# Optimization experiments

Hardware: AMD Instinct MI355X
Metric: run time of the kernel (lower is better)

## Reference

```python
import jax, jax.numpy as jnp
import numpy as np

MARGIN = 0.5
TAU = 0.25
RHO = 10.0
SEMIHARD_LOSS_THRESHOLD = 0.0
EPS = 1e-12


def _pairwise_cosine_distances(x):
    # L2-normalize rows, distances = 1 - cosine similarity  -> [N, N]
    xn = x / jnp.maximum(jnp.linalg.norm(x, axis=1, keepdims=True), EPS)
    sim = xn @ xn.T
    dist = 1.0 - sim
    return dist, sim, xn


def _source_similarities(src):
    # distances normalized by their batch mean ('relative' / avg distances)
    dist, sim, xn = _pairwise_cosine_distances(src)
    avg_dist = dist / jnp.maximum(jnp.mean(dist), EPS)
    return dist, avg_dist, sim, xn


def _weights_from_distances(avg_dist, tau):
    # soft relaxed label weights from teacher distances
    pair_weights = jnp.exp(-avg_dist / tau)                      # [N, N] pos-pair weight
    neg_pair_weights = 1.0 - pair_weights                        # [N, N]
    # triplet (i, j=pos, k=neg): weight = w_pos[i,j] * w_neg[i,k]  -> [N, N, N]
    triplet_weights = pair_weights[:, :, None] * neg_pair_weights[:, None, :]
    return pair_weights, neg_pair_weights, triplet_weights


def _safe_division(num, den):
    return jnp.where(den > 0.0, num / jnp.where(den > 0.0, den, 1.0), 0.0)


def setup_inputs() -> dict:
    key = jax.random.key(0)
    k1, k2 = jax.random.split(key)
    N, D = 384, 128
    source_embeddings = jax.random.normal(k1, (N, D), dtype=jnp.float32)
    embeddings = jax.random.normal(k2, (N, D), dtype=jnp.float32)
    return {"source_embeddings": source_embeddings, "embeddings": embeddings}


def reference(source_embeddings, embeddings):
    src = jax.lax.stop_gradient(source_embeddings)  # .detach()
    _, source_avg_distances, _, _ = _source_similarities(src)
    source_pair_weights, _, source_triplet_weights = _weights_from_distances(
        source_avg_distances, TAU)

    distances, _, _ = _pairwise_cosine_distances(embeddings)  # [N, N]
    # tdd[i, j, k] = d[i, k] - d[i, j]
    triplet_distance_differences = distances[:, None, :] - distances[:, :, None]
    triplet_losses = jax.nn.relu(MARGIN - triplet_distance_differences)  # [N, N, N]

    semihard = ((triplet_losses > 0.0) & (triplet_losses <= MARGIN)).astype(
        triplet_losses.dtype) * source_triplet_weights
    positive_pair_semihard_losses = jnp.max(triplet_losses * semihard, axis=2)  # [N, N]

    if SEMIHARD_LOSS_THRESHOLD > 0.0:
        hard = (triplet_losses > MARGIN).astype(triplet_losses.dtype) * source_triplet_weights
        normalized = jnp.min(triplet_losses - RHO * hard, axis=2)
        positive_pair_hard_losses = (normalized + RHO) * (normalized < 0.0).astype(
            normalized.dtype)
    else:
        positive_pair_hard_losses = 0.0

    gate = (positive_pair_semihard_losses <= SEMIHARD_LOSS_THRESHOLD).astype(
        positive_pair_semihard_losses.dtype)
    positive_pair_losses = positive_pair_semihard_losses + gate * positive_pair_hard_losses

    loss = _safe_division(jnp.sum(positive_pair_losses * source_pair_weights),
                          jnp.sum(source_pair_weights))
    return loss
```

## Files before the change

### kernel.cpp

```cpp
#include <hip/hip_runtime.h>
#include <hip/hip_bf16.h>

#define N 384
#define D 128
#define TAU 0.25f
#define MARGIN 0.5f

__global__ __launch_bounds__(256) void k_gram(const float* __restrict__ xsrc,
                                              const float* __restrict__ xemb,
                                              float* __restrict__ dsrc,
                                              float* __restrict__ demb,
                                              float* __restrict__ tsum,
                                              float* __restrict__ accum) {
    __shared__ float At[D][34];
    __shared__ float Bt[D][34];
    __shared__ float inv_s[64];
    __shared__ float ps[4];
    int bid = blockIdx.x;
    int lin = threadIdx.x;
    if (bid == 0 && lin == 0) {
        accum[0] = 0.f; accum[1] = 0.f;
        ((unsigned int*)accum)[2] = 0u;
    }
    int mat = (bid >= 144) ? 1 : 0;
    int t2  = mat ? bid - 144 : bid;
    int bi = t2 / 12, bj = t2 % 12;
    const float* xn = mat ? xemb : xsrc;
    float* out      = mat ? demb : dsrc;

    int wv = lin >> 6, lane = lin & 63;
    #pragma unroll
    for (int rr = 0; rr < 16; ++rr) {
        int vr = wv * 16 + rr;
        int r  = vr & 31;
        int grow = ((vr >> 5) ? bj : bi) * 32 + r;
        float2 v = ((const float2*)(xn + (size_t)grow * D))[lane];
        float ss = v.x * v.x + v.y * v.y;
        #pragma unroll
        for (int o = 32; o > 0; o >>= 1) ss += __shfl_xor(ss, o);
        if (lane == 0) inv_s[vr] = 1.0f / fmaxf(sqrtf(ss), 1e-12f);
    }
    __syncthreads();

    #pragma unroll
    for (int l = 0; l < 4; ++l) {
        int idx = lin + l * 256;
        int row = idx >> 5;
        int c4  = idx & 31;
        float ia = inv_s[row], ib = inv_s[32 + row];
        float4 va = ((const float4*)(xn + (size_t)(bi * 32 + row) * D))[c4];
        At[c4 * 4 + 0][row] = va.x * ia; At[c4 * 4 + 1][row] = va.y * ia;
        At[c4 * 4 + 2][row] = va.z * ia; At[c4 * 4 + 3][row] = va.w * ia;
        float4 vb = ((const float4*)(xn + (size_t)(bj * 32 + row) * D))[c4];
        Bt[c4 * 4 + 0][row] = vb.x * ib; Bt[c4 * 4 + 1][row] = vb.y * ib;
        Bt[c4 * 4 + 2][row] = vb.z * ib; Bt[c4 * 4 + 3][row] = vb.w * ib;
    }
    __syncthreads();

    int tx = lin & 15, ty = lin >> 4;
    float a00 = 0.f, a01 = 0.f, a10 = 0.f, a11 = 0.f;
    #pragma unroll 8
    for (int k = 0; k < D; k++) {
        float x0 = At[k][2 * ty], x1 = At[k][2 * ty + 1];
        float y0 = Bt[k][2 * tx], y1 = Bt[k][2 * tx + 1];
        a00 = fmaf(x0, y0, a00); a01 = fmaf(x0, y1, a01);
        a10 = fmaf(x1, y0, a10); a11 = fmaf(x1, y1, a11);
    }
    float d00 = 1.f - a00, d01 = 1.f - a01, d10 = 1.f - a10, d11 = 1.f - a11;
    int r0 = bi * 32 + 2 * ty, c0 = bj * 32 + 2 * tx;
    out[(size_t)r0 * N + c0]           = d00;
    out[(size_t)r0 * N + c0 + 1]       = d01;
    out[(size_t)(r0 + 1) * N + c0]     = d10;
    out[(size_t)(r0 + 1) * N + c0 + 1] = d11;

    if (!mat) {
        float s = d00 + d01 + d10 + d11;
        #pragma unroll
        for (int o = 32; o > 0; o >>= 1) s += __shfl_xor(s, o);
        if ((lin & 63) == 0) ps[lin >> 6] = s;
        __syncthreads();
        if (lin == 0) tsum[t2] = ps[0] + ps[1] + ps[2] + ps[3];
    }
}

__global__ __launch_bounds__(N) void k_main(const float* __restrict__ dsrc,
                                            const float* __restrict__ demb,
                                            const float* __restrict__ tsum,
                                            float* __restrict__ accum,
                                            float* __restrict__ out) {
    __shared__ float wn[N];
    __shared__ float pn[6], pd[6];
    int i = blockIdx.x;
    int t = threadIdx.x;
    float total = 0.f;
    #pragma unroll
    for (int j = 0; j < 144; ++j) total += tsum[j];
    float mean  = total * (1.0f / (float)(N * N));
    float scale = 1.0f / (fmaxf(mean, 1e-12f) * TAU);
    const float* dsr = dsrc + (size_t)i * N;
    const float* der = demb + (size_t)i * N;
    float w = expf(-dsr[t] * scale);
    wn[t] = 1.0f - w;
    float c = MARGIN + der[t];
    __syncthreads();
    float m0 = 0.f, m1 = 0.f, m2 = 0.f, m3 = 0.f;
    #pragma unroll 2
    for (int k = 0; k < N; k += 4) {
        float4 wvk = *(const float4*)&wn[k];
        float d0 = der[k], d1 = der[k + 1], d2 = der[k + 2], d3 = der[k + 3];
        float tl0 = c - d0; float v0 = tl0 * wvk.x;
        v0 = (tl0 <= MARGIN) ? v0 : 0.f; m0 = fmaxf(m0, v0);
        float tl1 = c - d1; float v1 = tl1 * wvk.y;
        v1 = (tl1 <= MARGIN) ? v1 : 0.f; m1 = fmaxf(m1, v1);
        float tl2 = c - d2; float v2 = tl2 * wvk.z;
        v2 = (tl2 <= MARGIN) ? v2 : 0.f; m2 = fmaxf(m2, v2);
        float tl3 = c - d3; float v3 = tl3 * wvk.w;
        v3 = (tl3 <= MARGIN) ? v3 : 0.f; m3 = fmaxf(m3, v3);
    }
    float m = fmaxf(fmaxf(m0, m1), fmaxf(m2, m3));
    float numc = w * w * m;
    float denc = w;
    #pragma unroll
    for (int o = 32; o > 0; o >>= 1) {
        numc += __shfl_xor(numc, o);
        denc += __shfl_xor(denc, o);
    }
    if ((t & 63) == 0) { pn[t >> 6] = numc; pd[t >> 6] = denc; }
    __syncthreads();
    if (t == 0) {
        float sn = 0.f, sd = 0.f;
        #pragma unroll
        for (int wv = 0; wv < 6; wv++) { sn += pn[wv]; sd += pd[wv]; }
        atomicAdd(&accum[0], sn);
        atomicAdd(&accum[1], sd);
        __threadfence();
        unsigned int tk = atomicAdd((unsigned int*)accum + 2, 1u);
        if (tk == (unsigned int)(N - 1)) {
            float num = atomicAdd(&accum[0], 0.f);
            float den = atomicAdd(&accum[1], 0.f);
            out[0] = (den > 0.f) ? num / den : 0.f;
        }
    }
}

extern "C" void kernel_launch(void* const* d_in, const int* in_sizes, int n_in,
                              void* d_out, int out_size, void* d_ws, size_t ws_size,
                              hipStream_t stream) {
    const float* src = (const float*)d_in[0];
    const float* emb = (const float*)d_in[1];
    float* out = (float*)d_out;

    float* ws = (float*)d_ws;
    float* dsrc  = ws;
    float* demb  = dsrc + N * N;
    float* tsum  = demb + N * N;
    float* accum = tsum + 144;

    k_gram<<<288, 256, 0, stream>>>(src, emb, dsrc, demb, tsum, accum);
    k_main<<<N, N, 0, stream>>>(dsrc, demb, tsum, accum, out);
}
```

Before: 94.42 us.

## Fuse gram and main kernels into one persistent kernel with grid barriers

Merges the two launches into a single 384-block kernel that uses software grid barriers between phases: row normalization written to workspace, tiled Gram/distance computation, a grid-wide pass writing exp weights, then the per-row semihard max reduction. This removes a kernel launch boundary and the redundant per-tile norm recomputation. In exchange it adds a hipMemsetAsync, three global spin barriers, and extra global round-trips for normalized rows and weights. The barrier relies on all 384 blocks being co-resident, which could deadlock if they are not.

```diff
diff --git a/kernel.cpp b/kernel.cpp
--- a/kernel.cpp
+++ b/kernel.cpp
@@ -5,140 +5,160 @@
 #define D 128
 #define TAU 0.25f
 #define MARGIN 0.5f
+#define NBLK 384
 
-__global__ __launch_bounds__(256) void k_gram(const float* __restrict__ xsrc,
-                                              const float* __restrict__ xemb,
-                                              float* __restrict__ dsrc,
-                                              float* __restrict__ demb,
-                                              float* __restrict__ tsum,
-                                              float* __restrict__ accum) {
-    __shared__ float At[D][34];
-    __shared__ float Bt[D][34];
-    __shared__ float inv_s[64];
-    __shared__ float ps[4];
-    int bid = blockIdx.x;
-    int lin = threadIdx.x;
-    if (bid == 0 && lin == 0) {
-        accum[0] = 0.f; accum[1] = 0.f;
-        ((unsigned int*)accum)[2] = 0u;
-    }
-    int mat = (bid >= 144) ? 1 : 0;
-    int t2  = mat ? bid - 144 : bid;
-    int bi = t2 / 12, bj = t2 % 12;
-    const float* xn = mat ? xemb : xsrc;
-    float* out      = mat ? demb : dsrc;
+struct GramSh { float At[D][34]; float Bt[D][34]; float ps[4]; };
+struct MainSh { float pn[6]; float pd[6]; };
+union ShU { GramSh g; MainSh m; };
 
-    int wv = lin >> 6, lane = lin & 63;
-    #pragma unroll
-    for (int rr = 0; rr < 16; ++rr) {
-        int vr = wv * 16 + rr;
-        int r  = vr & 31;
-        int grow = ((vr >> 5) ? bj : bi) * 32 + r;
-        float2 v = ((const float2*)(xn + (size_t)grow * D))[lane];
-        float ss = v.x * v.x + v.y * v.y;
-        #pragma unroll
-        for (int o = 32; o > 0; o >>= 1) ss += __shfl_xor(ss, o);
-        if (lane == 0) inv_s[vr] = 1.0f / fmaxf(sqrtf(ss), 1e-12f);
+__device__ __forceinline__ void grid_bar(unsigned* bar, unsigned target) {
+    __syncthreads();
+    if (threadIdx.x == 0) {
+        __threadfence();
+        atomicAdd(bar, 1u);
+        while (__hip_atomic_load(bar, __ATOMIC_RELAXED,
+                                 __HIP_MEMORY_SCOPE_AGENT) < target) {
+            __builtin_amdgcn_s_sleep(2);
+        }
+        __threadfence();
     }
     __syncthreads();
-
-    #pragma unroll
-    for (int l = 0; l < 4; ++l) {
-        int idx = lin + l * 256;
-        int row = idx >> 5;
-        int c4  = idx & 31;
-        float ia = inv_s[row], ib = inv_s[32 + row];
-        float4 va = ((const float4*)(xn + (size_t)(bi * 32 + row) * D))[c4];
-        At[c4 * 4 + 0][row] = va.x * ia; At[c4 * 4 + 1][row] = va.y * ia;
-        At[c4 * 4 + 2][row] = va.z * ia; At[c4 * 4 + 3][row] = va.w * ia;
-        float4 vb = ((const float4*)(xn + (size_t)(bj * 32 + row) * D))[c4];
-        Bt[c4 * 4 + 0][row] = vb.x * ib; Bt[c4 * 4 + 1][row] = vb.y * ib;
-        Bt[c4 * 4 + 2][row] = vb.z * ib; Bt[c4 * 4 + 3][row] = vb.w * ib;
-    }
-    __syncthreads();
-
-    int tx = lin & 15, ty = lin >> 4;
-    float a00 = 0.f, a01 = 0.f, a10 = 0.f, a11 = 0.f;
-    #pragma unroll 8
-    for (int k = 0; k < D; k++) {
-        float x0 = At[k][2 * ty], x1 = At[k][2 * ty + 1];
-        float y0 = Bt[k][2 * tx], y1 = Bt[k][2 * tx + 1];
-        a00 = fmaf(x0, y0, a00); a01 = fmaf(x0, y1, a01);
-        a10 = fmaf(x1, y0, a10); a11 = fmaf(x1, y1, a11);
-    }
-    float d00 = 1.f - a00, d01 = 1.f - a01, d10 = 1.f - a10, d11 = 1.f - a11;
-    int r0 = bi * 32 + 2 * ty, c0 = bj * 32 + 2 * tx;
-    out[(size_t)r0 * N + c0]           = d00;
-    out[(size_t)r0 * N + c0 + 1]       = d01;
-    out[(size_t)(r0 + 1) * N + c0]     = d10;
-    out[(size_t)(r0 + 1) * N + c0 + 1] = d11;
-
-    if (!mat) {
-        float s = d00 + d01 + d10 + d11;
-        #pragma unroll
-        for (int o = 32; o > 0; o >>= 1) s += __shfl_xor(s, o);
-        if ((lin & 63) == 0) ps[lin >> 6] = s;
-        __syncthreads();
-        if (lin == 0) tsum[t2] = ps[0] + ps[1] + ps[2] + ps[3];
-    }
 }
 
-__global__ __launch_bounds__(N) void k_main(const float* __restrict__ dsrc,
-                                            const float* __restrict__ demb,
-                                            const float* __restrict__ tsum,
-                                            float* __restrict__ accum,
-                                            float* __restrict__ out) {
-    __shared__ float wn[N];
-    __shared__ float pn[6], pd[6];
-    int i = blockIdx.x;
+__global__ __launch_bounds__(NBLK) void k_fused(const float* __restrict__ xsrc,
+                                                const float* __restrict__ xemb,
+                                                float* __restrict__ xn_src,
+                                                float* __restrict__ xn_emb,
+                                                float* __restrict__ dsrc,
+                                                float* __restrict__ demb,
+                                                float* __restrict__ wsrc,
+                                                float* __restrict__ tsum,
+                                                float* __restrict__ accum,
+                                                float* __restrict__ out) {
+    __shared__ ShU sh;
+    int bid = blockIdx.x;
     int t = threadIdx.x;
-    float total = 0.f;
-    #pragma unroll
-    for (int j = 0; j < 144; ++j) total += tsum[j];
-    float mean  = total * (1.0f / (float)(N * N));
-    float scale = 1.0f / (fmaxf(mean, 1e-12f) * TAU);
-    const float* dsr = dsrc + (size_t)i * N;
-    const float* der = demb + (size_t)i * N;
-    float w = expf(-dsr[t] * scale);
-    wn[t] = 1.0f - w;
-    float c = MARGIN + der[t];
-    __syncthreads();
-    float m0 = 0.f, m1 = 0.f, m2 = 0.f, m3 = 0.f;
-    #pragma unroll 2
-    for (int k = 0; k < N; k += 4) {
-        float4 wvk = *(const float4*)&wn[k];
-        float d0 = der[k], d1 = der[k + 1], d2 = der[k + 2], d3 = der[k + 3];
-        float tl0 = c - d0; float v0 = tl0 * wvk.x;
-        v0 = (tl0 <= MARGIN) ? v0 : 0.f; m0 = fmaxf(m0, v0);
-        float tl1 = c - d1; float v1 = tl1 * wvk.y;
-        v1 = (tl1 <= MARGIN) ? v1 : 0.f; m1 = fmaxf(m1, v1);
-        float tl2 = c - d2; float v2 = tl2 * wvk.z;
-        v2 = (tl2 <= MARGIN) ? v2 : 0.f; m2 = fmaxf(m2, v2);
-        float tl3 = c - d3; float v3 = tl3 * wvk.w;
-        v3 = (tl3 <= MARGIN) ? v3 : 0.f; m3 = fmaxf(m3, v3);
+    unsigned* bar = (unsigned*)(accum + 3);
+
+    {
+        int wv = t >> 6, lane = t & 63;
+        if (wv < 2) {
+            const float* x = wv ? xemb : xsrc;
+            float* y       = wv ? xn_emb : xn_src;
+            float2 v = ((const float2*)(x + (size_t)bid * D))[lane];
+            float ss = v.x * v.x + v.y * v.y;
+            #pragma unroll
+            for (int o = 32; o > 0; o >>= 1) ss += __shfl_xor(ss, o);
+            float inv = 1.0f / fmaxf(sqrtf(ss), 1e-12f);
+            float2 o2 = {v.x * inv, v.y * inv};
+            ((float2*)(y + (size_t)bid * D))[lane] = o2;
+        }
     }
-    float m = fmaxf(fmaxf(m0, m1), fmaxf(m2, m3));
-    float numc = w * w * m;
-    float denc = w;
-    #pragma unroll
-    for (int o = 32; o > 0; o >>= 1) {
-        numc += __shfl_xor(numc, o);
-        denc += __shfl_xor(denc, o);
+    grid_bar(bar, NBLK);
+
+    if (bid < 288) {
+        int mat = (bid >= 144) ? 1 : 0;
+        int t2  = mat ? bid - 144 : bid;
+        int bi = t2 / 12, bj = t2 % 12;
+        const float* xn = mat ? xn_emb : xn_src;
+        float* outm     = mat ? demb : dsrc;
+        if (t < 256) {
+            #pragma unroll
+            for (int l = 0; l < 4; ++l) {
+                int idx = t + l * 256;
+                int row = idx >> 5;
+                int c4  = idx & 31;
+                float4 va = ((const float4*)(xn + (size_t)(bi * 32 + row) * D))[c4];
+                sh.g.At[c4 * 4 + 0][row] = va.x; sh.g.At[c4 * 4 + 1][row] = va.y;
+                sh.g.At[c4 * 4 + 2][row] = va.z; sh.g.At[c4 * 4 + 3][row] = va.w;
+                float4 vb = ((const float4*)(xn + (size_t)(bj * 32 + row) * D))[c4];
+                sh.g.Bt[c4 * 4 + 0][row] = vb.x; sh.g.Bt[c4 * 4 + 1][row] = vb.y;
+                sh.g.Bt[c4 * 4 + 2][row] = vb.z; sh.g.Bt[c4 * 4 + 3][row] = vb.w;
+            }
+        }
+        __syncthreads();
+        float s_tile = 0.f;
+        if (t < 256) {
+            int tx = t & 15, ty = t >> 4;
+            float a00 = 0.f, a01 = 0.f, a10 = 0.f, a11 = 0.f;
+            #pragma unroll 8
+            for (int k = 0; k < D; k++) {
+                float x0 = sh.g.At[k][2 * ty], x1 = sh.g.At[k][2 * ty + 1];
+                float y0 = sh.g.Bt[k][2 * tx], y1 = sh.g.Bt[k][2 * tx + 1];
+                a00 = fmaf(x0, y0, a00); a01 = fmaf(x0, y1, a01);
+                a10 = fmaf(x1, y0, a10); a11 = fmaf(x1, y1, a11);
+            }
+            float d00 = 1.f - a00, d01 = 1.f - a01, d10 = 1.f - a10, d11 = 1.f - a11;
+            int r0 = bi * 32 + 2 * ty, c0 = bj * 32 + 2 * tx;
+            outm[(size_t)r0 * N + c0]           = d00;
+            outm[(size_t)r0 * N + c0 + 1]       = d01;
+            outm[(size_t)(r0 + 1) * N + c0]     = d10;
+            outm[(size_t)(r0 + 1) * N + c0 + 1] = d11;
+            if (!mat) s_tile = d00 + d01 + d10 + d11;
+        }
+        if (!mat) {
+            #pragma unroll
+            for (int o = 32; o > 0; o >>= 1) s_tile += __shfl_xor(s_tile, o);
+            if (t < 256 && (t & 63) == 0) sh.g.ps[t >> 6] = s_tile;
+            __syncthreads();
+            if (t == 0) tsum[t2] = sh.g.ps[0] + sh.g.ps[1] + sh.g.ps[2] + sh.g.ps[3];
+        }
     }
-    if ((t & 63) == 0) { pn[t >> 6] = numc; pd[t >> 6] = denc; }
-    __syncthreads();
-    if (t == 0) {
-        float sn = 0.f, sd = 0.f;
+    grid_bar(bar, 2 * NBLK);
+
+    {
+        float total = 0.f;
         #pragma unroll
-        for (int wv = 0; wv < 6; wv++) { sn += pn[wv]; sd += pd[wv]; }
-        atomicAdd(&accum[0], sn);
-        atomicAdd(&accum[1], sd);
-        __threadfence();
-        unsigned int tk = atomicAdd((unsigned int*)accum + 2, 1u);
-        if (tk == (unsigned int)(N - 1)) {
-            float num = atomicAdd(&accum[0], 0.f);
-            float den = atomicAdd(&accum[1], 0.f);
-            out[0] = (den > 0.f) ? num / den : 0.f;
+        for (int j = 0; j < 144; ++j) total += tsum[j];
+        float mean  = total * (1.0f / (float)(N * N));
+        float scale = 1.0f / (fmaxf(mean, 1e-12f) * TAU);
+        int idx = bid * N + t;
+        wsrc[idx] = expf(-dsrc[idx] * scale);
+    }
+    grid_bar(bar, 3 * NBLK);
+
+    {
+        const float* der = demb + (size_t)bid * N;
+        const float* wpr = wsrc + (size_t)bid * N;
+        float c = MARGIN + der[t];
+        float m0 = 0.f, m1 = 0.f, m2 = 0.f, m3 = 0.f;
+        #pragma unroll 2
+        for (int k = 0; k < N; k += 4) {
+            float d0 = der[k], d1 = der[k + 1], d2 = der[k + 2], d3 = der[k + 3];
+            float w0 = wpr[k], w1 = wpr[k + 1], w2 = wpr[k + 2], w3 = wpr[k + 3];
+            float tl0 = c - d0; float v0 = tl0 * (1.f - w0);
+            v0 = (tl0 <= MARGIN) ? v0 : 0.f; m0 = fmaxf(m0, v0);
+            float tl1 = c - d1; float v1 = tl1 * (1.f - w1);
+            v1 = (tl1 <= MARGIN) ? v1 : 0.f; m1 = fmaxf(m1, v1);
+            float tl2 = c - d2; float v2 = tl2 * (1.f - w2);
+            v2 = (tl2 <= MARGIN) ? v2 : 0.f; m2 = fmaxf(m2, v2);
+            float tl3 = c - d3; float v3 = tl3 * (1.f - w3);
+            v3 = (tl3 <= MARGIN) ? v3 : 0.f; m3 = fmaxf(m3, v3);
+        }
+        float m = fmaxf(fmaxf(m0, m1), fmaxf(m2, m3));
+        float w = wpr[t];
+        float numc = w * w * m;
+        float denc = w;
+        #pragma unroll
+        for (int o = 32; o > 0; o >>= 1) {
+            numc += __shfl_xor(numc, o);
+            denc += __shfl_xor(denc, o);
+        }
+        if ((t & 63) == 0) { sh.m.pn[t >> 6] = numc; sh.m.pd[t >> 6] = denc; }
+        __syncthreads();
+        if (t == 0) {
+            float sn = 0.f, sd = 0.f;
+            #pragma unroll
+            for (int wv = 0; wv < 6; wv++) { sn += sh.m.pn[wv]; sd += sh.m.pd[wv]; }
+            atomicAdd(&accum[0], sn);
+            atomicAdd(&accum[1], sd);
+            __threadfence();
+            unsigned tk = atomicAdd((unsigned*)(accum + 2), 1u);
+            if (tk == (unsigned)(NBLK - 1)) {
+                float num = atomicAdd(&accum[0], 0.f);
+                float den = atomicAdd(&accum[1], 0.f);
+                out[0] = (den > 0.f) ? num / den : 0.f;
+            }
         }
     }
 }
@@ -151,11 +171,15 @@
     float* out = (float*)d_out;
 
     float* ws = (float*)d_ws;
-    float* dsrc  = ws;
-    float* demb  = dsrc + N * N;
-    float* tsum  = demb + N * N;
-    float* accum = tsum + 144;
+    float* xn_src = ws;
+    float* xn_emb = xn_src + N * D;
+    float* dsrc   = xn_emb + N * D;
+    float* demb   = dsrc + N * N;
+    float* wsrc   = demb + N * N;
+    float* tsum   = wsrc + N * N;
+    float* accum  = tsum + 144;
 
-    k_gram<<<288, 256, 0, stream>>>(src, emb, dsrc, demb, tsum, accum);
-    k_main<<<N, N, 0, stream>>>(dsrc, demb, tsum, accum, out);
+    hipMemsetAsync(accum, 0, 4 * sizeof(float), stream);
+    k_fused<<<NBLK, NBLK, 0, stream>>>(src, emb, xn_src, xn_emb, dsrc, demb,
+                                       wsrc, tsum, accum, out);
 }
```

After: 201.5 us. +113.4%, slower.
